# Performance work log

Hardware: AMD Instinct MI355X
Metric: run time of the kernel (lower is better)

Reference implementation:

```python
import jax, jax.numpy as jnp
import numpy as np

N_NODES = 50000
NODE_DIM = 128
HIDDEN = 256
BLOCK_OUT = 128
NUM_CLASSES = 40
N_EDGES = 800000


def setup_inputs() -> dict:
    key = jax.random.key(0)
    ks = jax.random.split(key, 12)
    glorot = lambda k, fi, fo: jax.random.normal(k, (fi, fo), jnp.float32) * (2.0 / (fi + fo)) ** 0.5
    return {
        "x": jax.random.normal(ks[0], (N_NODES, NODE_DIM), jnp.float32),
        "edge_index": jax.random.randint(ks[1], (2, N_EDGES), 0, N_NODES, jnp.int64),
        # block1: Node2Edge MLP (2*node_dim -> hidden), Edge2Node MLP (hidden -> 128)
        "W1": glorot(ks[2], 2 * NODE_DIM, HIDDEN),
        "b1": jnp.zeros((HIDDEN,), jnp.float32),
        "W2": glorot(ks[3], HIDDEN, BLOCK_OUT),
        "b2": jnp.zeros((BLOCK_OUT,), jnp.float32),
        # final Node2Edge: Linear(2*128,128) -> ReLU -> Linear(128,num_classes) -> LogSoftmax
        "W3": glorot(ks[4], 2 * BLOCK_OUT, 128),
        "b3": jnp.zeros((128,), jnp.float32),
        "W4": glorot(ks[5], 128, NUM_CLASSES),
        "b4": jnp.zeros((NUM_CLASSES,), jnp.float32),
    }


def reference(x, edge_index, W1, b1, W2, b2, W3, b3, W4, b4):
    src, dst = edge_index[0], edge_index[1]
    # Node2Edge: gather endpoints, concat, edge MLP
    e = jnp.concatenate([x[src], x[dst]], axis=-1)          # [E, 2*node_dim]
    eh = jax.nn.relu(e @ W1 + b1)                            # [E, hidden]
    # Edge2Node: scatter-mean edge features to destination nodes
    agg = jax.ops.segment_sum(eh, dst, num_segments=N_NODES)
    cnt = jax.ops.segment_sum(jnp.ones((eh.shape[0],), eh.dtype), dst, num_segments=N_NODES)
    mean = agg / jnp.maximum(cnt, 1.0)[:, None]              # [N, hidden]
    h = jax.nn.relu(mean @ W2 + b2)                          # [N, 128]
    # final Node2Edge head -> per-edge class log-probs
    e2 = jnp.concatenate([h[src], h[dst]], axis=-1)          # [E, 256]
    z = jax.nn.relu(e2 @ W3 + b3)                            # [E, 128]
    logits = z @ W4 + b4                                     # [E, num_classes]
    return jax.nn.log_softmax(logits, axis=-1)
```

## Files before the change

### kernel.cpp

```cpp
#include <hip/hip_runtime.h>
#include <hip/hip_bf16.h>


typedef short bf16x8 __attribute__((ext_vector_type(8)));
typedef float f32x4 __attribute__((ext_vector_type(4)));

#define N_NODES 50000
#define N_EDGES 800000

__device__ __forceinline__ unsigned short f2bf(float f) {
  unsigned u = __builtin_bit_cast(unsigned, f);
  u = u + 0x7fffu + ((u >> 16) & 1u);
  return (unsigned short)(u >> 16);
}
__device__ __forceinline__ float lo_f(unsigned u) {
  return __builtin_bit_cast(float, u << 16);
}
__device__ __forceinline__ float hi_f(unsigned u) {
  return __builtin_bit_cast(float, u & 0xffff0000u);
}
__device__ __forceinline__ unsigned pack2(float lo, float hi) {
  return __builtin_amdgcn_perm(__builtin_bit_cast(unsigned, hi),
                               __builtin_bit_cast(unsigned, lo), 0x07060302u);
}
__device__ __forceinline__ int probe64(const int* ei) {
  return (ei[1] == 0 && ei[3] == 0 && ei[5] == 0 && ei[7] == 0) ? 1 : 0;
}
__device__ __forceinline__ int ld_src(const int* ei, int m64, int e) {
  return m64 ? ei[2 * e] : ei[e];
}
__device__ __forceinline__ int ld_dst(const int* ei, int m64, int e) {
  return m64 ? ei[2 * N_EDGES + 2 * e] : ei[N_EDGES + e];
}

__global__ void k_prep_frags(const float* __restrict__ W1, const float* __restrict__ W2,
                             const float* __restrict__ W3, const float* __restrict__ W4,
                             const float* __restrict__ b4,
                             unsigned short* __restrict__ w1f, unsigned short* __restrict__ w2f,
                             unsigned short* __restrict__ w3f, unsigned short* __restrict__ w4f,
                             float* __restrict__ b4p) {
  int gid = blockIdx.x * 256 + threadIdx.x;
  if (gid < 65536) {
    int i = gid & 7, lane = (gid >> 3) & 63, ks = (gid >> 9) & 3, ct = gid >> 11;
    int k = ks * 32 + (lane >> 4) * 8 + i;
    int c = ct * 16 + (lane & 15);
    float v = (c < 256) ? W1[k * 256 + c] : W1[(128 + k) * 256 + (c - 256)];
    w1f[gid] = f2bf(v);
  } else if (gid < 98304) {
    int f = gid - 65536;
    int i = f & 7, lane = (f >> 3) & 63, ks = (f >> 9) & 7, ct = f >> 12;
    int k = ks * 32 + (lane >> 4) * 8 + i;
    int c = ct * 16 + (lane & 15);
    w2f[f] = f2bf(W2[k * 128 + c]);
  } else if (gid < 131072) {
    int f = gid - 98304;
    int i = f & 7, lane = (f >> 3) & 63, ks = (f >> 9) & 3, ct = f >> 11;
    int k = ks * 32 + (lane >> 4) * 8 + i;
    int c = ct * 16 + (lane & 15);
    float v = (c < 128) ? W3[k * 128 + c] : W3[(128 + k) * 128 + (c - 128)];
    w3f[f] = f2bf(v);
  } else if (gid < 137216) {
    int f = gid - 131072;
    int i = f & 7, lane = (f >> 3) & 63, ks = (f >> 9) & 3, ct = f >> 11;
    int k = ks * 32 + (lane >> 4) * 8 + i;
    int c = ct * 16 + (lane & 15);
    w4f[f] = (c < 40) ? f2bf(W4[k * 40 + c]) : (unsigned short)0;
  } else if (gid < 137264) {
    int c = gid - 137216;
    b4p[c] = (c < 40) ? b4[c] : 0.f;
  }
}

__global__ void k_count_scatter(const int* __restrict__ ei, int* __restrict__ cnt,
                                unsigned short* __restrict__ pad) {
  int e = blockIdx.x * 256 + threadIdx.x;
  int m64 = probe64(ei);
  int s = ld_src(ei, m64, e), d = ld_dst(ei, m64, e);
  int pos = atomicAdd(&cnt[d], 1);
  pad[(d << 7) + pos] = (unsigned short)s;
}

__global__ __launch_bounds__(512, 2) void k_sy(const float* __restrict__ x,
                                               const unsigned short* __restrict__ w1f,
                                               const float* __restrict__ b1,
                                               unsigned short* __restrict__ S,
                                               unsigned short* __restrict__ Ypr) {
  __shared__ __attribute__((aligned(16))) short A[64 * 128];
  const int t = threadIdx.x;
  const int nb = blockIdx.x * 64;
  const int nv = min(64, N_NODES - nb);
  const int w = t >> 6, l = t & 63, lr = l & 15, lh = l >> 4;

  bf16x8 B[4][4];
#pragma unroll
  for (int ci = 0; ci < 4; ++ci)
#pragma unroll
    for (int ks = 0; ks < 4; ++ks)
      B[ci][ks] = *(const bf16x8*)(w1f + (((w * 4 + ci) * 4 + ks) * 64 + l) * 8);

#pragma unroll
  for (int j = 0; j < 2; ++j) {
    int c = t + 512 * j;
    int row = c >> 4, ck = c & 15;
    int rr = (row < nv) ? row : 0;
    const float* gp = x + (long)(nb + rr) * 128 + ck * 8;
    float4 v0 = *(const float4*)gp;
    float4 v1 = *(const float4*)(gp + 4);
    bf16x8 o;
    o[0] = (short)f2bf(v0.x); o[1] = (short)f2bf(v0.y);
    o[2] = (short)f2bf(v0.z); o[3] = (short)f2bf(v0.w);
    o[4] = (short)f2bf(v1.x); o[5] = (short)f2bf(v1.y);
    o[6] = (short)f2bf(v1.z); o[7] = (short)f2bf(v1.w);
    int off = (row << 8) + (ck << 4);
    off ^= (row & 7) << 4;
    *(bf16x8*)((char*)A + off) = o;
  }
  __syncthreads();

#pragma unroll
  for (int rt = 0; rt < 4; ++rt) {
    f32x4 acc[4] = {};
#pragma unroll
    for (int ks = 0; ks < 4; ++ks) {
      int row = rt * 16 + lr;
      int off = (row << 8) + (ks << 6) + (lh << 4);
      off ^= (row & 7) << 4;
      bf16x8 a = *(const bf16x8*)((const char*)A + off);
#pragma unroll
      for (int ci = 0; ci < 4; ++ci)
        acc[ci] = __builtin_amdgcn_mfma_f32_16x16x32_bf16(a, B[ci][ks], acc[ci], 0, 0, 0);
    }
#pragma unroll
    for (int ci = 0; ci < 4; ++ci) {
      int col = (w * 4 + ci) * 16 + lr;
#pragma unroll
      for (int r = 0; r < 4; ++r) {
        int row = rt * 16 + lh * 4 + r;
        if (row < nv) {
          if (col < 256) {
            S[(long)(nb + row) * 256 + col] = f2bf(acc[ci][r]);
          } else {
            Ypr[(long)(nb + row) * 256 + (col - 256)] = f2bf(acc[ci][r] + b1[col - 256]);
          }
        }
      }
    }
  }
}

__global__ __launch_bounds__(512) void k_edge_agg(const unsigned short* __restrict__ S,
                                                  unsigned short* __restrict__ Ypr,
                                                  const int* __restrict__ cnt,
                                                  const unsigned short* __restrict__ pad) {
  const int t = threadIdx.x, w = t >> 6, l = t & 63;
  const int d = blockIdx.x * 8 + w;
  const int n = cnt[d];
  const unsigned short* lp = pad + (d << 7);
  unsigned short* Yp = Ypr + (long)d * 256 + l * 4;
  const uint2 yu = *(const uint2*)Yp;
  const float y0 = lo_f(yu.x), y1 = hi_f(yu.x), y2 = lo_f(yu.y), y3 = hi_f(yu.y);
  float a0 = 0.f, a1 = 0.f, a2 = 0.f, a3 = 0.f;
  int pos = 0;
  for (; pos + 8 <= n; pos += 8) {
    uint2 u[8];
#pragma unroll
    for (int j = 0; j < 8; ++j) {
      int s = (int)lp[pos + j];
      u[j] = *(const uint2*)(S + (long)s * 256 + l * 4);
    }
#pragma unroll
    for (int j = 0; j < 8; ++j) {
      a0 += fmaxf(lo_f(u[j].x) + y0, 0.f);
      a1 += fmaxf(hi_f(u[j].x) + y1, 0.f);
      a2 += fmaxf(lo_f(u[j].y) + y2, 0.f);
      a3 += fmaxf(hi_f(u[j].y) + y3, 0.f);
    }
  }
  for (; pos < n; ++pos) {
    int s = (int)lp[pos];
    uint2 uA = *(const uint2*)(S + (long)s * 256 + l * 4);
    a0 += fmaxf(lo_f(uA.x) + y0, 0.f);
    a1 += fmaxf(hi_f(uA.x) + y1, 0.f);
    a2 += fmaxf(lo_f(uA.y) + y2, 0.f);
    a3 += fmaxf(hi_f(uA.y) + y3, 0.f);
  }
  float inv = 1.0f / fmaxf((float)n, 1.0f);
  ushort4 o;
  o.x = f2bf(a0 * inv); o.y = f2bf(a1 * inv);
  o.z = f2bf(a2 * inv); o.w = f2bf(a3 * inv);
  *(ushort4*)Yp = o;
}

__global__ __launch_bounds__(256, 2) void k_pq(const unsigned short* __restrict__ Ypr,
                                               unsigned short* __restrict__ PQ,
                                               const unsigned short* __restrict__ w2f,
                                               const float* __restrict__ b2,
                                               const unsigned short* __restrict__ w3f,
                                               const float* __restrict__ b3) {
  __shared__ __attribute__((aligned(16))) short M[64 * 256];
  __shared__ __attribute__((aligned(16))) short H[64 * 128];
  const int t = threadIdx.x;
  const int nb = blockIdx.x * 64;
  const int nv = min(64, N_NODES - nb);
  const int w = t >> 6, l = t & 63, lr = l & 15, lh = l >> 4;

  bf16x8 B2[2][8];
#pragma unroll
  for (int ci = 0; ci < 2; ++ci)
#pragma unroll
    for (int ks = 0; ks < 8; ++ks)
      B2[ci][ks] = *(const bf16x8*)(w2f + (((w * 2 + ci) * 8 + ks) * 64 + l) * 8);

#pragma unroll
  for (int j = 0; j < 8; ++j) {
    int c = t + 256 * j;
    int row = c >> 5, ck = c & 31;
    int rr = (row < nv) ? row : 0;
    int4 v = *(const int4*)(Ypr + (long)(nb + rr) * 256 + ck * 8);
    int off = (row << 9) + (ck << 4);
    off ^= (row & 7) << 4;
    *(int4*)((char*)M + off) = v;
  }
  __syncthreads();

#pragma unroll
  for (int rt = 0; rt < 4; ++rt) {
    f32x4 acc[2] = {};
#pragma unroll
    for (int ks = 0; ks < 8; ++ks) {
      int row = rt * 16 + lr;
      int off = (row << 9) + (ks << 6) + (lh << 4);
      off ^= (row & 7) << 4;
      bf16x8 a = *(const bf16x8*)((const char*)M + off);
      acc[0] = __builtin_amdgcn_mfma_f32_16x16x32_bf16(a, B2[0][ks], acc[0], 0, 0, 0);
      acc[1] = __builtin_amdgcn_mfma_f32_16x16x32_bf16(a, B2[1][ks], acc[1], 0, 0, 0);
    }
#pragma unroll
    for (int ci = 0; ci < 2; ++ci) {
      int col = (w * 2 + ci) * 16 + lr;
      float bb = b2[col];
#pragma unroll
      for (int r = 0; r < 4; ++r) {
        int row = rt * 16 + lh * 4 + r;
        int off = (row << 8) + (col << 1);
        off ^= (row & 7) << 4;
        *(short*)((char*)H + off) = (short)f2bf(fmaxf(acc[ci][r] + bb, 0.f));
      }
    }
  }
  __syncthreads();

  bf16x8 B3[4][4];
#pragma unroll
  for (int ci = 0; ci < 4; ++ci)
#pragma unroll
    for (int ks = 0; ks < 4; ++ks)
      B3[ci][ks] = *(const bf16x8*)(w3f + (((w * 4 + ci) * 4 + ks) * 64 + l) * 8);

#pragma unroll
  for (int rt = 0; rt < 4; ++rt) {
    f32x4 acc[4] = {};
#pragma unroll
    for (int ks = 0; ks < 4; ++ks) {
      int row = rt * 16 + lr;
      int off = (row << 8) + (ks << 6) + (lh << 4);
      off ^= (row & 7) << 4;
      bf16x8 a = *(const bf16x8*)((const char*)H + off);
#pragma unroll
      for (int ci = 0; ci < 4; ++ci)
        acc[ci] = __builtin_amdgcn_mfma_f32_16x16x32_bf16(a, B3[ci][ks], acc[ci], 0, 0, 0);
    }
#pragma unroll
    for (int ci = 0; ci < 4; ++ci) {
      int col = (w * 4 + ci) * 16 + lr;
      float bb = (col >= 128) ? b3[col - 128] : 0.f;
#pragma unroll
      for (int r = 0; r < 4; ++r) {
        int row = rt * 16 + lh * 4 + r;
        if (row < nv) PQ[(long)(nb + row) * 256 + col] = f2bf(acc[ci][r] + bb);
      }
    }
  }
}

__global__ __launch_bounds__(256) void k_head(const unsigned short* __restrict__ PQ,
                                              const int* __restrict__ ei,
                                              const unsigned short* __restrict__ w4f,
                                              const float* __restrict__ b4p,
                                              float* __restrict__ out) {
  const int t = threadIdx.x, w = t >> 6, l = t & 63, lr = l & 15, lh = l >> 4;
  const int m64 = probe64(ei);
  const int eb = blockIdx.x * 128 + w * 32;
  const int elA = eb + lr;
  const int elB = eb + 16 + lr;
  const int snA = ld_src(ei, m64, elA), dnA = ld_dst(ei, m64, elA);
  const int snB = ld_src(ei, m64, elB), dnB = ld_dst(ei, m64, elB);
  const unsigned short* PpA = PQ + (long)snA * 256;
  const unsigned short* QpA = PQ + (long)dnA * 256 + 128;
  const unsigned short* PpB = PQ + (long)snB * 256;
  const unsigned short* QpB = PQ + (long)dnB * 256 + 128;

  bf16x8 B4[3][4];
#pragma unroll
  for (int ci = 0; ci < 3; ++ci)
#pragma unroll
    for (int ks = 0; ks < 4; ++ks)
      B4[ci][ks] = *(const bf16x8*)(w4f + ((ci * 4 + ks) * 64 + l) * 8);

  f32x4 accA[3] = {};
  f32x4 accB[3] = {};
#pragma unroll
  for (int ks = 0; ks < 4; ++ks) {
    uint4 puA = *(const uint4*)(PpA + ks * 32 + lh * 8);
    uint4 quA = *(const uint4*)(QpA + ks * 32 + lh * 8);
    uint4 puB = *(const uint4*)(PpB + ks * 32 + lh * 8);
    uint4 quB = *(const uint4*)(QpB + ks * 32 + lh * 8);
    int4 a4A, a4B;
    a4A.x = pack2(fmaxf(lo_f(puA.x) + lo_f(quA.x), 0.f), fmaxf(hi_f(puA.x) + hi_f(quA.x), 0.f));
    a4A.y = pack2(fmaxf(lo_f(puA.y) + lo_f(quA.y), 0.f), fmaxf(hi_f(puA.y) + hi_f(quA.y), 0.f));
    a4A.z = pack2(fmaxf(lo_f(puA.z) + lo_f(quA.z), 0.f), fmaxf(hi_f(puA.z) + hi_f(quA.z), 0.f));
    a4A.w = pack2(fmaxf(lo_f(puA.w) + lo_f(quA.w), 0.f), fmaxf(hi_f(puA.w) + hi_f(quA.w), 0.f));
    a4B.x = pack2(fmaxf(lo_f(puB.x) + lo_f(quB.x), 0.f), fmaxf(hi_f(puB.x) + hi_f(quB.x), 0.f));
    a4B.y = pack2(fmaxf(lo_f(puB.y) + lo_f(quB.y), 0.f), fmaxf(hi_f(puB.y) + hi_f(quB.y), 0.f));
    a4B.z = pack2(fmaxf(lo_f(puB.z) + lo_f(quB.z), 0.f), fmaxf(hi_f(puB.z) + hi_f(quB.z), 0.f));
    a4B.w = pack2(fmaxf(lo_f(puB.w) + lo_f(quB.w), 0.f), fmaxf(hi_f(puB.w) + hi_f(quB.w), 0.f));
    bf16x8 aA = __builtin_bit_cast(bf16x8, a4A);
    bf16x8 aB = __builtin_bit_cast(bf16x8, a4B);
#pragma unroll
    for (int ci = 0; ci < 3; ++ci) {
      accA[ci] = __builtin_amdgcn_mfma_f32_16x16x32_bf16(aA, B4[ci][ks], accA[ci], 0, 0, 0);
      accB[ci] = __builtin_amdgcn_mfma_f32_16x16x32_bf16(aB, B4[ci][ks], accB[ci], 0, 0, 0);
    }
  }

  const bool val2 = lr < 8;
  const float bb0 = b4p[lr], bb1 = b4p[16 + lr], bb2 = b4p[32 + lr];
#pragma unroll
  for (int es = 0; es < 2; ++es) {
    float lg0[4], lg1[4], lg2[4];
#pragma unroll
    for (int r = 0; r < 4; ++r) {
      f32x4* ac = es ? accB : accA;
      lg0[r] = ac[0][r] + bb0;
      lg1[r] = ac[1][r] + bb1;
      lg2[r] = ac[2][r] + bb2;
    }
#pragma unroll
    for (int r = 0; r < 4; ++r) {
      float m = fmaxf(lg0[r], lg1[r]);
      if (val2) m = fmaxf(m, lg2[r]);
      m = fmaxf(m, __shfl_xor(m, 1, 64));
      m = fmaxf(m, __shfl_xor(m, 2, 64));
      m = fmaxf(m, __shfl_xor(m, 4, 64));
      m = fmaxf(m, __shfl_xor(m, 8, 64));
      float s = __expf(lg0[r] - m) + __expf(lg1[r] - m) + (val2 ? __expf(lg2[r] - m) : 0.f);
      s += __shfl_xor(s, 1, 64);
      s += __shfl_xor(s, 2, 64);
      s += __shfl_xor(s, 4, 64);
      s += __shfl_xor(s, 8, 64);
      float lse = m + __logf(s);
      long ob = (long)(eb + es * 16 + lh * 4 + r) * 40;
      out[ob + lr] = lg0[r] - lse;
      out[ob + 16 + lr] = lg1[r] - lse;
      if (val2) out[ob + 32 + lr] = lg2[r] - lse;
    }
  }
}

extern "C" void kernel_launch(void* const* d_in, const int* in_sizes, int n_in,
                              void* d_out, int out_size, void* d_ws, size_t ws_size,
                              hipStream_t stream) {
  const float* x = (const float*)d_in[0];
  const int* ei = (const int*)d_in[1];
  const float* W1 = (const float*)d_in[2];
  const float* b1 = (const float*)d_in[3];
  const float* W2 = (const float*)d_in[4];
  const float* b2 = (const float*)d_in[5];
  const float* W3 = (const float*)d_in[6];
  const float* b3 = (const float*)d_in[7];
  const float* W4 = (const float*)d_in[8];
  const float* b4 = (const float*)d_in[9];
  char* ws = (char*)d_ws;
  int* cnt = (int*)(ws + 0);
  unsigned short* pad = (unsigned short*)(ws + 200064);
  unsigned short* S = (unsigned short*)(ws + 13000192);
  unsigned short* Ypr = (unsigned short*)(ws + 38600192);
  unsigned short* w1f = (unsigned short*)(ws + 64200192);
  unsigned short* w2f = (unsigned short*)(ws + 64331264);
  unsigned short* w3f = (unsigned short*)(ws + 64396800);
  unsigned short* w4f = (unsigned short*)(ws + 64462336);
  float* b4p = (float*)(ws + 64474624);
  float* out = (float*)d_out;

  (void)hipMemsetAsync(ws, 0, 200064, stream);
  k_prep_frags<<<537, 256, 0, stream>>>(W1, W2, W3, W4, b4, w1f, w2f, w3f, w4f, b4p);
  k_count_scatter<<<3125, 256, 0, stream>>>(ei, cnt, pad);
  k_sy<<<782, 512, 0, stream>>>(x, w1f, b1, S, Ypr);
  k_edge_agg<<<6250, 512, 0, stream>>>(S, Ypr, cnt, pad);
  k_pq<<<782, 256, 0, stream>>>(Ypr, S, w2f, b2, w3f, b3);
  k_head<<<6250, 256, 0, stream>>>(S, ei, w4f, b4p, out);
}
```

Baseline: 274.1 us.

## Gather fp8-compressed PQ table in head kernel and merge prep with scatter

Adds a conversion pass that packs the bf16 per-node P/Q table into fp8, so the per-edge head kernel gathers half as many bytes per endpoint. The head kernel now handles 64 edges per wave instead of 32, giving more loads in flight per thread. The weight-fragment prep kernel and the count/scatter kernel are merged into one launch. In exchange there is an extra pass over the table, a loss of precision from fp8 storage of the hidden pre-activations, and higher register pressure in the head kernel.

```diff
diff --git a/kernel.cpp b/kernel.cpp
--- a/kernel.cpp
+++ b/kernel.cpp
@@ -4,6 +4,7 @@
 
 typedef short bf16x8 __attribute__((ext_vector_type(8)));
 typedef float f32x4 __attribute__((ext_vector_type(4)));
+typedef float f32x2 __attribute__((ext_vector_type(2)));
 
 #define N_NODES 50000
 #define N_EDGES 800000
@@ -33,13 +34,23 @@
   return m64 ? ei[2 * N_EDGES + 2 * e] : ei[N_EDGES + e];
 }
 
-__global__ void k_prep_frags(const float* __restrict__ W1, const float* __restrict__ W2,
-                             const float* __restrict__ W3, const float* __restrict__ W4,
-                             const float* __restrict__ b4,
-                             unsigned short* __restrict__ w1f, unsigned short* __restrict__ w2f,
-                             unsigned short* __restrict__ w3f, unsigned short* __restrict__ w4f,
-                             float* __restrict__ b4p) {
-  int gid = blockIdx.x * 256 + threadIdx.x;
+__global__ void k_prep_scatter(const float* __restrict__ W1, const float* __restrict__ W2,
+                               const float* __restrict__ W3, const float* __restrict__ W4,
+                               const float* __restrict__ b4,
+                               unsigned short* __restrict__ w1f, unsigned short* __restrict__ w2f,
+                               unsigned short* __restrict__ w3f, unsigned short* __restrict__ w4f,
+                               float* __restrict__ b4p, const int* __restrict__ ei,
+                               int* __restrict__ cnt, unsigned short* __restrict__ pad) {
+  const int t = threadIdx.x;
+  if (blockIdx.x >= 537) {
+    int e = (blockIdx.x - 537) * 256 + t;
+    int m64 = probe64(ei);
+    int s = ld_src(ei, m64, e), d = ld_dst(ei, m64, e);
+    int pos = atomicAdd(&cnt[d], 1);
+    pad[(d << 7) + pos] = (unsigned short)s;
+    return;
+  }
+  int gid = blockIdx.x * 256 + t;
   if (gid < 65536) {
     int i = gid & 7, lane = (gid >> 3) & 63, ks = (gid >> 9) & 3, ct = gid >> 11;
     int k = ks * 32 + (lane >> 4) * 8 + i;
@@ -71,15 +82,6 @@
   }
 }
 
-__global__ void k_count_scatter(const int* __restrict__ ei, int* __restrict__ cnt,
-                                unsigned short* __restrict__ pad) {
-  int e = blockIdx.x * 256 + threadIdx.x;
-  int m64 = probe64(ei);
-  int s = ld_src(ei, m64, e), d = ld_dst(ei, m64, e);
-  int pos = atomicAdd(&cnt[d], 1);
-  pad[(d << 7) + pos] = (unsigned short)s;
-}
-
 __global__ __launch_bounds__(512, 2) void k_sy(const float* __restrict__ x,
                                                const unsigned short* __restrict__ w1f,
                                                const float* __restrict__ b1,
@@ -283,22 +285,35 @@
   }
 }
 
-__global__ __launch_bounds__(256) void k_head(const unsigned short* __restrict__ PQ,
+__global__ void k_cvt(const unsigned short* __restrict__ PQ, unsigned char* __restrict__ PQ8) {
+  long i = ((long)blockIdx.x * 256 + threadIdx.x) * 8;
+  uint4 v = *(const uint4*)(PQ + i);
+  int r0 = __builtin_amdgcn_cvt_pk_fp8_f32(lo_f(v.x), hi_f(v.x), 0, false);
+  r0 = __builtin_amdgcn_cvt_pk_fp8_f32(lo_f(v.y), hi_f(v.y), r0, true);
+  int r1 = __builtin_amdgcn_cvt_pk_fp8_f32(lo_f(v.z), hi_f(v.z), 0, false);
+  r1 = __builtin_amdgcn_cvt_pk_fp8_f32(lo_f(v.w), hi_f(v.w), r1, true);
+  uint2 o;
+  o.x = (unsigned)r0;
+  o.y = (unsigned)r1;
+  *(uint2*)(PQ8 + i) = o;
+}
+
+__global__ __launch_bounds__(256) void k_head(const unsigned char* __restrict__ PQ8,
                                               const int* __restrict__ ei,
                                               const unsigned short* __restrict__ w4f,
                                               const float* __restrict__ b4p,
                                               float* __restrict__ out) {
   const int t = threadIdx.x, w = t >> 6, l = t & 63, lr = l & 15, lh = l >> 4;
   const int m64 = probe64(ei);
-  const int eb = blockIdx.x * 128 + w * 32;
-  const int elA = eb + lr;
-  const int elB = eb + 16 + lr;
-  const int snA = ld_src(ei, m64, elA), dnA = ld_dst(ei, m64, elA);
-  const int snB = ld_src(ei, m64, elB), dnB = ld_dst(ei, m64, elB);
-  const unsigned short* PpA = PQ + (long)snA * 256;
-  const unsigned short* QpA = PQ + (long)dnA * 256 + 128;
-  const unsigned short* PpB = PQ + (long)snB * 256;
-  const unsigned short* QpB = PQ + (long)dnB * 256 + 128;
+  const int eb = blockIdx.x * 256 + w * 64;
+
+  long pbase[4], qbase[4];
+#pragma unroll
+  for (int c = 0; c < 4; ++c) {
+    int e = eb + c * 16 + lr;
+    pbase[c] = (long)ld_src(ei, m64, e) * 256 + lh * 8;
+    qbase[c] = (long)ld_dst(ei, m64, e) * 256 + 128 + lh * 8;
+  }
 
   bf16x8 B4[3][4];
 #pragma unroll
@@ -307,43 +322,43 @@
     for (int ks = 0; ks < 4; ++ks)
       B4[ci][ks] = *(const bf16x8*)(w4f + ((ci * 4 + ks) * 64 + l) * 8);
 
-  f32x4 accA[3] = {};
-  f32x4 accB[3] = {};
+  f32x4 acc[4][3] = {};
 #pragma unroll
   for (int ks = 0; ks < 4; ++ks) {
-    uint4 puA = *(const uint4*)(PpA + ks * 32 + lh * 8);
-    uint4 quA = *(const uint4*)(QpA + ks * 32 + lh * 8);
-    uint4 puB = *(const uint4*)(PpB + ks * 32 + lh * 8);
-    uint4 quB = *(const uint4*)(QpB + ks * 32 + lh * 8);
-    int4 a4A, a4B;
-    a4A.x = pack2(fmaxf(lo_f(puA.x) + lo_f(quA.x), 0.f), fmaxf(hi_f(puA.x) + hi_f(quA.x), 0.f));
-    a4A.y = pack2(fmaxf(lo_f(puA.y) + lo_f(quA.y), 0.f), fmaxf(hi_f(puA.y) + hi_f(quA.y), 0.f));
-    a4A.z = pack2(fmaxf(lo_f(puA.z) + lo_f(quA.z), 0.f), fmaxf(hi_f(puA.z) + hi_f(quA.z), 0.f));
-    a4A.w = pack2(fmaxf(lo_f(puA.w) + lo_f(quA.w), 0.f), fmaxf(hi_f(puA.w) + hi_f(quA.w), 0.f));
-    a4B.x = pack2(fmaxf(lo_f(puB.x) + lo_f(quB.x), 0.f), fmaxf(hi_f(puB.x) + hi_f(quB.x), 0.f));
-    a4B.y = pack2(fmaxf(lo_f(puB.y) + lo_f(quB.y), 0.f), fmaxf(hi_f(puB.y) + hi_f(quB.y), 0.f));
-    a4B.z = pack2(fmaxf(lo_f(puB.z) + lo_f(quB.z), 0.f), fmaxf(hi_f(puB.z) + hi_f(quB.z), 0.f));
-    a4B.w = pack2(fmaxf(lo_f(puB.w) + lo_f(quB.w), 0.f), fmaxf(hi_f(puB.w) + hi_f(quB.w), 0.f));
-    bf16x8 aA = __builtin_bit_cast(bf16x8, a4A);
-    bf16x8 aB = __builtin_bit_cast(bf16x8, a4B);
-#pragma unroll
-    for (int ci = 0; ci < 3; ++ci) {
-      accA[ci] = __builtin_amdgcn_mfma_f32_16x16x32_bf16(aA, B4[ci][ks], accA[ci], 0, 0, 0);
-      accB[ci] = __builtin_amdgcn_mfma_f32_16x16x32_bf16(aB, B4[ci][ks], accB[ci], 0, 0, 0);
+#pragma unroll
+    for (int c = 0; c < 4; ++c) {
+      uint2 p8 = *(const uint2*)(PQ8 + pbase[c] + ks * 32);
+      uint2 q8 = *(const uint2*)(PQ8 + qbase[c] + ks * 32);
+      f32x2 p01 = __builtin_amdgcn_cvt_pk_f32_fp8(p8.x, false);
+      f32x2 p23 = __builtin_amdgcn_cvt_pk_f32_fp8(p8.x, true);
+      f32x2 p45 = __builtin_amdgcn_cvt_pk_f32_fp8(p8.y, false);
+      f32x2 p67 = __builtin_amdgcn_cvt_pk_f32_fp8(p8.y, true);
+      f32x2 q01 = __builtin_amdgcn_cvt_pk_f32_fp8(q8.x, false);
+      f32x2 q23 = __builtin_amdgcn_cvt_pk_f32_fp8(q8.x, true);
+      f32x2 q45 = __builtin_amdgcn_cvt_pk_f32_fp8(q8.y, false);
+      f32x2 q67 = __builtin_amdgcn_cvt_pk_f32_fp8(q8.y, true);
+      int4 a4;
+      a4.x = pack2(fmaxf(p01[0] + q01[0], 0.f), fmaxf(p01[1] + q01[1], 0.f));
+      a4.y = pack2(fmaxf(p23[0] + q23[0], 0.f), fmaxf(p23[1] + q23[1], 0.f));
+      a4.z = pack2(fmaxf(p45[0] + q45[0], 0.f), fmaxf(p45[1] + q45[1], 0.f));
+      a4.w = pack2(fmaxf(p67[0] + q67[0], 0.f), fmaxf(p67[1] + q67[1], 0.f));
+      bf16x8 a = __builtin_bit_cast(bf16x8, a4);
+#pragma unroll
+      for (int ci = 0; ci < 3; ++ci)
+        acc[c][ci] = __builtin_amdgcn_mfma_f32_16x16x32_bf16(a, B4[ci][ks], acc[c][ci], 0, 0, 0);
     }
   }
 
   const bool val2 = lr < 8;
   const float bb0 = b4p[lr], bb1 = b4p[16 + lr], bb2 = b4p[32 + lr];
 #pragma unroll
-  for (int es = 0; es < 2; ++es) {
+  for (int c = 0; c < 4; ++c) {
     float lg0[4], lg1[4], lg2[4];
 #pragma unroll
     for (int r = 0; r < 4; ++r) {
-      f32x4* ac = es ? accB : accA;
-      lg0[r] = ac[0][r] + bb0;
-      lg1[r] = ac[1][r] + bb1;
-      lg2[r] = ac[2][r] + bb2;
+      lg0[r] = acc[c][0][r] + bb0;
+      lg1[r] = acc[c][1][r] + bb1;
+      lg2[r] = acc[c][2][r] + bb2;
     }
 #pragma unroll
     for (int r = 0; r < 4; ++r) {
@@ -359,7 +374,7 @@
       s += __shfl_xor(s, 4, 64);
       s += __shfl_xor(s, 8, 64);
       float lse = m + __logf(s);
-      long ob = (long)(eb + es * 16 + lh * 4 + r) * 40;
+      long ob = (long)(eb + c * 16 + lh * 4 + r) * 40;
       out[ob + lr] = lg0[r] - lse;
       out[ob + 16 + lr] = lg1[r] - lse;
       if (val2) out[ob + 32 + lr] = lg2[r] - lse;
@@ -390,13 +405,15 @@
   unsigned short* w3f = (unsigned short*)(ws + 64396800);
   unsigned short* w4f = (unsigned short*)(ws + 64462336);
   float* b4p = (float*)(ws + 64474624);
+  unsigned char* PQ8 = (unsigned char*)(ws + 64475136);
   float* out = (float*)d_out;
 
   (void)hipMemsetAsync(ws, 0, 200064, stream);
-  k_prep_frags<<<537, 256, 0, stream>>>(W1, W2, W3, W4, b4, w1f, w2f, w3f, w4f, b4p);
-  k_count_scatter<<<3125, 256, 0, stream>>>(ei, cnt, pad);
+  k_prep_scatter<<<3662, 256, 0, stream>>>(W1, W2, W3, W4, b4, w1f, w2f, w3f, w4f, b4p,
+                                           ei, cnt, pad);
   k_sy<<<782, 512, 0, stream>>>(x, w1f, b1, S, Ypr);
   k_edge_agg<<<6250, 512, 0, stream>>>(S, Ypr, cnt, pad);
   k_pq<<<782, 256, 0, stream>>>(Ypr, S, w2f, b2, w3f, b3);
-  k_head<<<6250, 256, 0, stream>>>(S, ei, w4f, b4p, out);
-}
+  k_cvt<<<6250, 256, 0, stream>>>(S, PQ8);
+  k_head<<<3125, 256, 0, stream>>>(PQ8, ei, w4f, b4p, out);
+}
```

Measured after the change: 289.7 us. 5.7% more time.
